# Optimization experiments

Measured on AMD Instinct MI355X. Metric: run time of the kernel, lower is better.

The kernel has to match this reference:

```python
import math
import jax, jax.numpy as jnp
import numpy as np

N_QO_HEADS = 32
N_KV_HEADS = 8
HEAD_DIM = 128
PAGE = 16          # tokens per cache block
NUM_BLOCKS = 512   # total blocks in KV cache
B = 2              # num sequences
SEQ = 2048         # tokens per sequence (q_len == kv_len, prefill)
T = B * SEQ        # total tokens


def setup_inputs() -> dict:
    key = jax.random.key(0)
    ks = jax.random.split(key, 5)
    query = jax.random.normal(ks[0], (T, N_QO_HEADS * HEAD_DIM), dtype=jnp.float32)
    k_new = jax.random.normal(ks[1], (T, N_KV_HEADS * HEAD_DIM), dtype=jnp.float32)
    v_new = jax.random.normal(ks[2], (T, N_KV_HEADS * HEAD_DIM), dtype=jnp.float32)
    key_cache = jax.random.normal(ks[3], (NUM_BLOCKS, PAGE, N_KV_HEADS, HEAD_DIM), dtype=jnp.float32)
    value_cache = jax.random.normal(ks[4], (NUM_BLOCKS, PAGE, N_KV_HEADS, HEAD_DIM), dtype=jnp.float32)
    nb = SEQ // PAGE
    block_tables = jnp.arange(B * nb, dtype=jnp.int32).reshape(B, nb)
    new_cache_slots = jnp.arange(T, dtype=jnp.int32)  # consistent with block_tables
    return {
        'query': query, 'key': k_new, 'value': v_new,
        'key_cache': key_cache, 'value_cache': value_cache,
        'block_tables': block_tables, 'new_cache_slots': new_cache_slots,
    }


def reference(query, key, value, key_cache, value_cache, block_tables, new_cache_slots):
    T_, _ = query.shape
    q = query.reshape(T_, N_QO_HEADS, HEAD_DIM)
    k_new = key.reshape(T_, N_KV_HEADS, HEAD_DIM)
    v_new = value.reshape(T_, N_KV_HEADS, HEAD_DIM)

    # set_kv_cache: scatter new K/V into the paged cache at new_cache_slots
    kc = key_cache.reshape(NUM_BLOCKS * PAGE, N_KV_HEADS, HEAD_DIM).at[new_cache_slots].set(k_new)
    vc = value_cache.reshape(NUM_BLOCKS * PAGE, N_KV_HEADS, HEAD_DIM).at[new_cache_slots].set(v_new)

    # paged gather: per-sequence token indices from block tables
    nb = block_tables.shape[1]
    idx = (block_tables[:, :, None] * PAGE + jnp.arange(PAGE, dtype=jnp.int32)[None, None, :]).reshape(B, SEQ)
    k = kc[idx]  # [B, S, Hkv, d]
    v = vc[idx]  # [B, S, Hkv, d]

    g = N_QO_HEADS // N_KV_HEADS
    qb = q.reshape(B, SEQ, N_KV_HEADS, g, HEAD_DIM)
    sm_scale = 1.0 / math.sqrt(HEAD_DIM)
    scores = jnp.einsum('bqhgd,bkhd->bhgqk', qb, k) * sm_scale  # [B,Hkv,g,S,S]

    # causal mask (q_len == kv_len so mask is k > q)
    causal = jnp.tril(jnp.ones((SEQ, SEQ), dtype=bool))
    scores = jnp.where(causal, scores, -jnp.inf)
    p = jax.nn.softmax(scores, axis=-1)
    o = jnp.einsum('bhgqk,bkhd->bqhgd', p, v)  # [B,S,Hkv,g,d]
    out = o.reshape(T_, N_QO_HEADS * HEAD_DIM).astype(query.dtype)
    return out
```

## Files before the change

### kernel.cpp

```cpp
#include <hip/hip_runtime.h>
#include <cstdint>

#define HQ 32
#define HKV 8
#define D 128
#define PAGE 16
#define SEQB 2048
#define NB 2
#define NBT (SEQB/PAGE)
#define NSLOTS (512*16)

#define BM 32
#define BN 64

typedef __bf16 bf16;
typedef __bf16 bf16x8 __attribute__((ext_vector_type(8)));
typedef float  f32x4  __attribute__((ext_vector_type(4)));

typedef __attribute__((address_space(3))) uint32_t lds_u32_t;
typedef __attribute__((address_space(1))) uint32_t glb_u32_t;

__device__ __forceinline__ void gload16(const bf16* g, bf16* l) {
    __builtin_amdgcn_global_load_lds((const glb_u32_t*)g, (lds_u32_t*)l, 16, 0, 0);
}

__global__ __launch_bounds__(256) void build_inv(const int* __restrict__ slots,
                                                 int* __restrict__ inv) {
    int t = blockIdx.x * 256 + threadIdx.x;
    if (t < NB * SEQB) inv[slots[t]] = t;
}

__global__ __launch_bounds__(256) void pack_kv(
    const float* __restrict__ knew, const float* __restrict__ vnew,
    const float* __restrict__ kc,   const float* __restrict__ vc,
    const int* __restrict__ btab,   const int* __restrict__ inv,
    bf16* __restrict__ Kp, bf16* __restrict__ Vp)
{
    int gid = blockIdx.x;
    if (gid < 2048) {
        int i   = gid*256 + threadIdx.x;
        int d8  = i & 15;
        int sg  = (i >> 4) & (SEQB - 1);
        int hkv = (i >> 15) & 7;
        int b   = i >> 18;
        int phys = btab[b*NBT + (sg >> 4)] * PAGE + (sg & 15);
        int t    = inv[phys];
        const float* src = (t >= 0 ? knew + (size_t)t * (HKV*D)
                                   : kc   + (size_t)phys * (HKV*D)) + hkv*D + d8*8;
        float4 f0 = *(const float4*)src;
        float4 f1 = *(const float4*)(src + 4);
        bf16x8 o;
        o[0]=(bf16)f0.x; o[1]=(bf16)f0.y; o[2]=(bf16)f0.z; o[3]=(bf16)f0.w;
        o[4]=(bf16)f1.x; o[5]=(bf16)f1.y; o[6]=(bf16)f1.z; o[7]=(bf16)f1.w;
        *(bf16x8*)(Kp + ((size_t)(b*HKV + hkv)*SEQB + sg)*D + d8*8) = o;
    } else {
        int i   = (gid - 2048)*256 + threadIdx.x;
        int d   = i & 127;
        int tg  = (i >> 7) & 255;
        int hkv = (i >> 15) & 7;
        int b   = i >> 18;
        int base = (tg >> 3) * 64 + ((tg >> 2) & 1) * 32 + (tg & 3) * 4;
        bf16x8 o;
        #pragma unroll
        for (int u = 0; u < 8; ++u) {
            int sg   = base + (u & 3) + ((u >> 2) << 4);
            int phys = btab[b*NBT + (sg >> 4)] * PAGE + (sg & 15);
            int t    = inv[phys];
            float v = (t >= 0) ? vnew[(size_t)t * (HKV*D) + hkv*D + d]
                               : vc  [(size_t)phys * (HKV*D) + hkv*D + d];
            o[u] = (bf16)v;
        }
        *(bf16x8*)(Vp + ((size_t)(b*HKV + hkv)*D + d)*SEQB + tg*8) = o;
    }
}

__global__ __launch_bounds__(256, 2) void attn(
    const float* __restrict__ q,
    const bf16* __restrict__ Kp,
    const bf16* __restrict__ Vp,
    float* __restrict__ out)
{
    __shared__ bf16 KT[2][BN * D];
    __shared__ bf16 VT[2][BN * D];

    const int hkv = blockIdx.x >> 5;
    const int vq  = blockIdx.x & 31;
    const int b   = blockIdx.y;

    const int tid  = threadIdx.x;
    const int w    = tid >> 6;
    const int lane = tid & 63;
    const int c    = lane & 15;
    const int quad = lane >> 4;
    const int hq   = hkv*4 + w;

    const bf16* Kbase = Kp + (size_t)(b*HKV + hkv) * SEQB * D;
    const bf16* Vbase = Vp + (size_t)(b*HKV + hkv) * (size_t)D * SEQB;

    const float CS = 0.08838834764831845f * 1.4426950408889634f;

    int kgo[4], vgo[4];
    #pragma unroll
    for (int it = 0; it < 4; ++it) {
        int o   = tid + it*256;
        int tok = o >> 4, sl = o & 15;
        int g   = (sl & 8) | ((sl & 7) ^ (tok & 7));
        kgo[it] = tok*D + g*8;
        int d = o >> 3, s2 = o & 7;
        int tg = s2 ^ (d & 7);
        vgo[it] = d*SEQB + tg*8;
    }

    int cur = 0;
    #pragma unroll
    for (int it = 0; it < 4; ++it) gload16(Kbase + kgo[it], &KT[0][(tid + it*256)*8]);
    #pragma unroll
    for (int it = 0; it < 4; ++it) gload16(Vbase + vgo[it], &VT[0][(tid + it*256)*8]);

    #pragma unroll 1
    for (int pass = 0; pass < 2; ++pass) {
        const int qt = pass ? vq : 63 - vq;

        bf16x8 qf[2][4];
        #pragma unroll
        for (int u = 0; u < 2; ++u) {
            const float* qrow = q + (size_t)(b*SEQB + qt*BM + u*16 + c) * (HQ*D) + hq*D;
            #pragma unroll
            for (int kk = 0; kk < 4; ++kk) {
                float4 f0 = *(const float4*)(qrow + kk*32 + quad*8);
                float4 f1 = *(const float4*)(qrow + kk*32 + quad*8 + 4);
                bf16x8 a;
                a[0]=(bf16)(f0.x*CS); a[1]=(bf16)(f0.y*CS); a[2]=(bf16)(f0.z*CS); a[3]=(bf16)(f0.w*CS);
                a[4]=(bf16)(f1.x*CS); a[5]=(bf16)(f1.y*CS); a[6]=(bf16)(f1.z*CS); a[7]=(bf16)(f1.w*CS);
                qf[u][kk] = a;
            }
        }

        float lrun[2];
        f32x4 accO[2][8];
        lrun[0] = 0.f; lrun[1] = 0.f;
        #pragma unroll
        for (int u = 0; u < 2; ++u)
            #pragma unroll
            for (int dt = 0; dt < 8; ++dt) accO[u][dt] = (f32x4){0.f,0.f,0.f,0.f};

        const int jmax  = (qt*BM + BM - 1) >> 6;
        const int qrow0 = qt*BM + c;

        for (int j = 0; j <= jmax; ++j) {
            __syncthreads();

            if (j < jmax) {
                const bf16* kgp = Kbase + (size_t)(j+1)*BN*D;
                const bf16* vgp = Vbase + (j+1)*BN;
                #pragma unroll
                for (int it = 0; it < 4; ++it) gload16(kgp + kgo[it], &KT[cur^1][(tid + it*256)*8]);
                #pragma unroll
                for (int it = 0; it < 4; ++it) gload16(vgp + vgo[it], &VT[cur^1][(tid + it*256)*8]);
            } else if (pass == 0) {
                #pragma unroll
                for (int it = 0; it < 4; ++it) gload16(Kbase + kgo[it], &KT[cur^1][(tid + it*256)*8]);
                #pragma unroll
                for (int it = 0; it < 4; ++it) gload16(Vbase + vgo[it], &VT[cur^1][(tid + it*256)*8]);
            }

            const bf16* Kt = KT[cur];
            const bf16* Vt = VT[cur];
            const int kb0  = j * BN;
            const bool diag = (j == jmax);

            uint32_t pw[2][4][2];
            #pragma unroll
            for (int nt = 0; nt < 4; ++nt) {
                const int tok = nt*16 + c;
                f32x4 s0 = (f32x4){0.f,0.f,0.f,0.f};
                f32x4 s1 = (f32x4){0.f,0.f,0.f,0.f};
                __builtin_amdgcn_s_setprio(1);
                #pragma unroll
                for (int kk = 0; kk < 4; ++kk) {
                    int sl = ((kk & 2) << 2) | (((kk & 1) * 4 + quad) ^ (tok & 7));
                    bf16x8 kb = *(const bf16x8*)(Kt + tok*D + sl*8);
                    s0 = __builtin_amdgcn_mfma_f32_16x16x32_bf16(kb, qf[0][kk], s0, 0, 0, 0);
                    s1 = __builtin_amdgcn_mfma_f32_16x16x32_bf16(kb, qf[1][kk], s1, 0, 0, 0);
                }
                __builtin_amdgcn_s_setprio(0);
                const int tokg = kb0 + nt*16 + quad*4;
                #pragma unroll
                for (int u = 0; u < 2; ++u) {
                    f32x4 sv = u ? s1 : s0;
                    float p0 = __builtin_amdgcn_exp2f(sv[0]);
                    float p1 = __builtin_amdgcn_exp2f(sv[1]);
                    float p2 = __builtin_amdgcn_exp2f(sv[2]);
                    float p3 = __builtin_amdgcn_exp2f(sv[3]);
                    if (diag) {
                        const int qr = qrow0 + u*16;
                        if (tokg     > qr) p0 = 0.0f;
                        if (tokg + 1 > qr) p1 = 0.0f;
                        if (tokg + 2 > qr) p2 = 0.0f;
                        if (tokg + 3 > qr) p3 = 0.0f;
                    }
                    lrun[u] += (p0 + p1) + (p2 + p3);
                    asm("v_cvt_pk_bf16_f32 %0, %1, %2" : "=v"(pw[u][nt][0]) : "v"(p0), "v"(p1));
                    asm("v_cvt_pk_bf16_f32 %0, %1, %2" : "=v"(pw[u][nt][1]) : "v"(p2), "v"(p3));
                }
            }

            union PA { uint32_t w[4]; bf16x8 v; };
            PA pa00, pa01, pa10, pa11;
            pa00.w[0]=pw[0][0][0]; pa00.w[1]=pw[0][0][1]; pa00.w[2]=pw[0][1][0]; pa00.w[3]=pw[0][1][1];
            pa01.w[0]=pw[0][2][0]; pa01.w[1]=pw[0][2][1]; pa01.w[2]=pw[0][3][0]; pa01.w[3]=pw[0][3][1];
            pa10.w[0]=pw[1][0][0]; pa10.w[1]=pw[1][0][1]; pa10.w[2]=pw[1][1][0]; pa10.w[3]=pw[1][1][1];
            pa11.w[0]=pw[1][2][0]; pa11.w[1]=pw[1][2][1]; pa11.w[2]=pw[1][3][0]; pa11.w[3]=pw[1][3][1];
            const int sl0 = ((quad    ) ^ (c & 7)) * 8;
            const int sl1 = ((quad + 4) ^ (c & 7)) * 8;
            __builtin_amdgcn_s_setprio(1);
            #pragma unroll
            for (int dt = 0; dt < 8; ++dt) {
                const bf16* vrow = Vt + (size_t)(dt*16 + c) * BN;
                bf16x8 vb0 = *(const bf16x8*)(vrow + sl0);
                accO[0][dt] = __builtin_amdgcn_mfma_f32_16x16x32_bf16(pa00.v, vb0, accO[0][dt], 0, 0, 0);
                accO[1][dt] = __builtin_amdgcn_mfma_f32_16x16x32_bf16(pa10.v, vb0, accO[1][dt], 0, 0, 0);
                bf16x8 vb1 = *(const bf16x8*)(vrow + sl1);
                accO[0][dt] = __builtin_amdgcn_mfma_f32_16x16x32_bf16(pa01.v, vb1, accO[0][dt], 0, 0, 0);
                accO[1][dt] = __builtin_amdgcn_mfma_f32_16x16x32_bf16(pa11.v, vb1, accO[1][dt], 0, 0, 0);
            }
            __builtin_amdgcn_s_setprio(0);

            cur ^= 1;
        }

        #pragma unroll
        for (int u = 0; u < 2; ++u) {
            float l = lrun[u];
            l += __shfl_xor(l, 16);
            l += __shfl_xor(l, 32);
            #pragma unroll
            for (int rr = 0; rr < 4; ++rr) {
                float lr = __shfl(l, quad*4 + rr);
                float inv = 1.0f / lr;
                float* orow = out + (size_t)(b*SEQB + qt*BM + u*16 + quad*4 + rr) * (HQ*D) + hq*D;
                #pragma unroll
                for (int dt = 0; dt < 8; ++dt)
                    orow[dt*16 + c] = accO[u][dt][rr] * inv;
            }
        }
    }
}

extern "C" void kernel_launch(void* const* d_in, const int* in_sizes, int n_in,
                              void* d_out, int out_size, void* d_ws, size_t ws_size,
                              hipStream_t stream) {
    const float* q     = (const float*)d_in[0];
    const float* knew  = (const float*)d_in[1];
    const float* vnew  = (const float*)d_in[2];
    const float* kc    = (const float*)d_in[3];
    const float* vc    = (const float*)d_in[4];
    const int*   btab  = (const int*)d_in[5];
    const int*   slots = (const int*)d_in[6];
    float*       out   = (float*)d_out;

    int*  inv = (int*)d_ws;
    bf16* Kp  = (bf16*)((char*)d_ws + 65536);
    bf16* Vp  = Kp + (size_t)NB * HKV * SEQB * D;

    hipMemsetAsync(inv, 0xFF, NSLOTS * sizeof(int), stream);
    build_inv<<<(NB*SEQB + 255)/256, 256, 0, stream>>>(slots, inv);
    pack_kv<<<4096, 256, 0, stream>>>(knew, vnew, kc, vc, btab, inv, Kp, Vp);

    dim3 grid(8 * 32, NB);
    attn<<<grid, 256, 0, stream>>>(q, Kp, Vp, out);
}
```

Measured before the change: 257.9 us.

## Single-buffer K in LDS, one q-tile per block, raise occupancy to 3

K drops to a single LDS buffer while V keeps two. The next K/V load is issued only after the QK^T phase, behind explicit vmcnt waits and raw barriers. The two-pass pairing of q-tiles per block is removed: the grid doubles to one q-tile per block, ordered longest-first with heads interleaved. Launch bounds ask for 3 blocks per CU. The aim is more resident blocks and better load balance, at the cost of less prefetch distance for K and possible register pressure.

```diff
diff --git a/kernel.cpp b/kernel.cpp
--- a/kernel.cpp
+++ b/kernel.cpp
@@ -74,17 +74,17 @@
     }
 }
 
-__global__ __launch_bounds__(256, 2) void attn(
+__global__ __launch_bounds__(256, 3) void attn(
     const float* __restrict__ q,
     const bf16* __restrict__ Kp,
     const bf16* __restrict__ Vp,
     float* __restrict__ out)
 {
-    __shared__ bf16 KT[2][BN * D];
+    __shared__ bf16 Kt[BN * D];
     __shared__ bf16 VT[2][BN * D];
 
-    const int hkv = blockIdx.x >> 5;
-    const int vq  = blockIdx.x & 31;
+    const int hkv = blockIdx.x & 7;
+    const int qt  = 63 - (blockIdx.x >> 3);
     const int b   = blockIdx.y;
 
     const int tid  = threadIdx.x;
@@ -111,138 +111,134 @@
         vgo[it] = d*SEQB + tg*8;
     }
 
-    int cur = 0;
-    #pragma unroll
-    for (int it = 0; it < 4; ++it) gload16(Kbase + kgo[it], &KT[0][(tid + it*256)*8]);
+    #pragma unroll
+    for (int it = 0; it < 4; ++it) gload16(Kbase + kgo[it], &Kt[(tid + it*256)*8]);
     #pragma unroll
     for (int it = 0; it < 4; ++it) gload16(Vbase + vgo[it], &VT[0][(tid + it*256)*8]);
 
-    #pragma unroll 1
-    for (int pass = 0; pass < 2; ++pass) {
-        const int qt = pass ? vq : 63 - vq;
-
-        bf16x8 qf[2][4];
-        #pragma unroll
-        for (int u = 0; u < 2; ++u) {
-            const float* qrow = q + (size_t)(b*SEQB + qt*BM + u*16 + c) * (HQ*D) + hq*D;
+    bf16x8 qf[2][4];
+    #pragma unroll
+    for (int u = 0; u < 2; ++u) {
+        const float* qrow = q + (size_t)(b*SEQB + qt*BM + u*16 + c) * (HQ*D) + hq*D;
+        #pragma unroll
+        for (int kk = 0; kk < 4; ++kk) {
+            float4 f0 = *(const float4*)(qrow + kk*32 + quad*8);
+            float4 f1 = *(const float4*)(qrow + kk*32 + quad*8 + 4);
+            bf16x8 a;
+            a[0]=(bf16)(f0.x*CS); a[1]=(bf16)(f0.y*CS); a[2]=(bf16)(f0.z*CS); a[3]=(bf16)(f0.w*CS);
+            a[4]=(bf16)(f1.x*CS); a[5]=(bf16)(f1.y*CS); a[6]=(bf16)(f1.z*CS); a[7]=(bf16)(f1.w*CS);
+            qf[u][kk] = a;
+        }
+    }
+
+    float lrun[2];
+    f32x4 accO[2][8];
+    lrun[0] = 0.f; lrun[1] = 0.f;
+    #pragma unroll
+    for (int u = 0; u < 2; ++u)
+        #pragma unroll
+        for (int dt = 0; dt < 8; ++dt) accO[u][dt] = (f32x4){0.f,0.f,0.f,0.f};
+
+    const int jmax  = (qt*BM + BM - 1) >> 6;
+    const int qrow0 = qt*BM + c;
+    int vcur = 0;
+
+    for (int j = 0; j <= jmax; ++j) {
+        asm volatile("s_waitcnt vmcnt(4)" ::: "memory");
+        __builtin_amdgcn_s_barrier();
+        __builtin_amdgcn_sched_barrier(0);
+
+        const int kb0  = j * BN;
+        const bool diag = (j == jmax);
+
+        uint32_t pw[2][4][2];
+        #pragma unroll
+        for (int nt = 0; nt < 4; ++nt) {
+            const int tok = nt*16 + c;
+            f32x4 s0 = (f32x4){0.f,0.f,0.f,0.f};
+            f32x4 s1 = (f32x4){0.f,0.f,0.f,0.f};
+            __builtin_amdgcn_s_setprio(1);
             #pragma unroll
             for (int kk = 0; kk < 4; ++kk) {
-                float4 f0 = *(const float4*)(qrow + kk*32 + quad*8);
-                float4 f1 = *(const float4*)(qrow + kk*32 + quad*8 + 4);
-                bf16x8 a;
-                a[0]=(bf16)(f0.x*CS); a[1]=(bf16)(f0.y*CS); a[2]=(bf16)(f0.z*CS); a[3]=(bf16)(f0.w*CS);
-                a[4]=(bf16)(f1.x*CS); a[5]=(bf16)(f1.y*CS); a[6]=(bf16)(f1.z*CS); a[7]=(bf16)(f1.w*CS);
-                qf[u][kk] = a;
-            }
-        }
-
-        float lrun[2];
-        f32x4 accO[2][8];
-        lrun[0] = 0.f; lrun[1] = 0.f;
-        #pragma unroll
-        for (int u = 0; u < 2; ++u)
-            #pragma unroll
-            for (int dt = 0; dt < 8; ++dt) accO[u][dt] = (f32x4){0.f,0.f,0.f,0.f};
-
-        const int jmax  = (qt*BM + BM - 1) >> 6;
-        const int qrow0 = qt*BM + c;
-
-        for (int j = 0; j <= jmax; ++j) {
-            __syncthreads();
-
-            if (j < jmax) {
-                const bf16* kgp = Kbase + (size_t)(j+1)*BN*D;
-                const bf16* vgp = Vbase + (j+1)*BN;
-                #pragma unroll
-                for (int it = 0; it < 4; ++it) gload16(kgp + kgo[it], &KT[cur^1][(tid + it*256)*8]);
-                #pragma unroll
-                for (int it = 0; it < 4; ++it) gload16(vgp + vgo[it], &VT[cur^1][(tid + it*256)*8]);
-            } else if (pass == 0) {
-                #pragma unroll
-                for (int it = 0; it < 4; ++it) gload16(Kbase + kgo[it], &KT[cur^1][(tid + it*256)*8]);
-                #pragma unroll
-                for (int it = 0; it < 4; ++it) gload16(Vbase + vgo[it], &VT[cur^1][(tid + it*256)*8]);
-            }
-
-            const bf16* Kt = KT[cur];
-            const bf16* Vt = VT[cur];
-            const int kb0  = j * BN;
-            const bool diag = (j == jmax);
-
-            uint32_t pw[2][4][2];
-            #pragma unroll
-            for (int nt = 0; nt < 4; ++nt) {
-                const int tok = nt*16 + c;
-                f32x4 s0 = (f32x4){0.f,0.f,0.f,0.f};
-                f32x4 s1 = (f32x4){0.f,0.f,0.f,0.f};
-                __builtin_amdgcn_s_setprio(1);
-                #pragma unroll
-                for (int kk = 0; kk < 4; ++kk) {
-                    int sl = ((kk & 2) << 2) | (((kk & 1) * 4 + quad) ^ (tok & 7));
-                    bf16x8 kb = *(const bf16x8*)(Kt + tok*D + sl*8);
-                    s0 = __builtin_amdgcn_mfma_f32_16x16x32_bf16(kb, qf[0][kk], s0, 0, 0, 0);
-                    s1 = __builtin_amdgcn_mfma_f32_16x16x32_bf16(kb, qf[1][kk], s1, 0, 0, 0);
-                }
-                __builtin_amdgcn_s_setprio(0);
-                const int tokg = kb0 + nt*16 + quad*4;
-                #pragma unroll
-                for (int u = 0; u < 2; ++u) {
-                    f32x4 sv = u ? s1 : s0;
-                    float p0 = __builtin_amdgcn_exp2f(sv[0]);
-                    float p1 = __builtin_amdgcn_exp2f(sv[1]);
-                    float p2 = __builtin_amdgcn_exp2f(sv[2]);
-                    float p3 = __builtin_amdgcn_exp2f(sv[3]);
-                    if (diag) {
-                        const int qr = qrow0 + u*16;
-                        if (tokg     > qr) p0 = 0.0f;
-                        if (tokg + 1 > qr) p1 = 0.0f;
-                        if (tokg + 2 > qr) p2 = 0.0f;
-                        if (tokg + 3 > qr) p3 = 0.0f;
-                    }
-                    lrun[u] += (p0 + p1) + (p2 + p3);
-                    asm("v_cvt_pk_bf16_f32 %0, %1, %2" : "=v"(pw[u][nt][0]) : "v"(p0), "v"(p1));
-                    asm("v_cvt_pk_bf16_f32 %0, %1, %2" : "=v"(pw[u][nt][1]) : "v"(p2), "v"(p3));
-                }
-            }
-
-            union PA { uint32_t w[4]; bf16x8 v; };
-            PA pa00, pa01, pa10, pa11;
-            pa00.w[0]=pw[0][0][0]; pa00.w[1]=pw[0][0][1]; pa00.w[2]=pw[0][1][0]; pa00.w[3]=pw[0][1][1];
-            pa01.w[0]=pw[0][2][0]; pa01.w[1]=pw[0][2][1]; pa01.w[2]=pw[0][3][0]; pa01.w[3]=pw[0][3][1];
-            pa10.w[0]=pw[1][0][0]; pa10.w[1]=pw[1][0][1]; pa10.w[2]=pw[1][1][0]; pa10.w[3]=pw[1][1][1];
-            pa11.w[0]=pw[1][2][0]; pa11.w[1]=pw[1][2][1]; pa11.w[2]=pw[1][3][0]; pa11.w[3]=pw[1][3][1];
-            const int sl0 = ((quad    ) ^ (c & 7)) * 8;
-            const int sl1 = ((quad + 4) ^ (c & 7)) * 8;
-            __builtin_amdgcn_s_setprio(1);
-            #pragma unroll
-            for (int dt = 0; dt < 8; ++dt) {
-                const bf16* vrow = Vt + (size_t)(dt*16 + c) * BN;
-                bf16x8 vb0 = *(const bf16x8*)(vrow + sl0);
-                accO[0][dt] = __builtin_amdgcn_mfma_f32_16x16x32_bf16(pa00.v, vb0, accO[0][dt], 0, 0, 0);
-                accO[1][dt] = __builtin_amdgcn_mfma_f32_16x16x32_bf16(pa10.v, vb0, accO[1][dt], 0, 0, 0);
-                bf16x8 vb1 = *(const bf16x8*)(vrow + sl1);
-                accO[0][dt] = __builtin_amdgcn_mfma_f32_16x16x32_bf16(pa01.v, vb1, accO[0][dt], 0, 0, 0);
-                accO[1][dt] = __builtin_amdgcn_mfma_f32_16x16x32_bf16(pa11.v, vb1, accO[1][dt], 0, 0, 0);
+                int sl = ((kk & 2) << 2) | (((kk & 1) * 4 + quad) ^ (tok & 7));
+                bf16x8 kb = *(const bf16x8*)(Kt + tok*D + sl*8);
+                s0 = __builtin_amdgcn_mfma_f32_16x16x32_bf16(kb, qf[0][kk], s0, 0, 0, 0);
+                s1 = __builtin_amdgcn_mfma_f32_16x16x32_bf16(kb, qf[1][kk], s1, 0, 0, 0);
             }
             __builtin_amdgcn_s_setprio(0);
-
-            cur ^= 1;
-        }
-
-        #pragma unroll
-        for (int u = 0; u < 2; ++u) {
-            float l = lrun[u];
-            l += __shfl_xor(l, 16);
-            l += __shfl_xor(l, 32);
-            #pragma unroll
-            for (int rr = 0; rr < 4; ++rr) {
-                float lr = __shfl(l, quad*4 + rr);
-                float inv = 1.0f / lr;
-                float* orow = out + (size_t)(b*SEQB + qt*BM + u*16 + quad*4 + rr) * (HQ*D) + hq*D;
-                #pragma unroll
-                for (int dt = 0; dt < 8; ++dt)
-                    orow[dt*16 + c] = accO[u][dt][rr] * inv;
+            const int tokg = kb0 + nt*16 + quad*4;
+            #pragma unroll
+            for (int u = 0; u < 2; ++u) {
+                f32x4 sv = u ? s1 : s0;
+                float p0 = __builtin_amdgcn_exp2f(sv[0]);
+                float p1 = __builtin_amdgcn_exp2f(sv[1]);
+                float p2 = __builtin_amdgcn_exp2f(sv[2]);
+                float p3 = __builtin_amdgcn_exp2f(sv[3]);
+                if (diag) {
+                    const int qr = qrow0 + u*16;
+                    if (tokg     > qr) p0 = 0.0f;
+                    if (tokg + 1 > qr) p1 = 0.0f;
+                    if (tokg + 2 > qr) p2 = 0.0f;
+                    if (tokg + 3 > qr) p3 = 0.0f;
+                }
+                lrun[u] += (p0 + p1) + (p2 + p3);
+                asm("v_cvt_pk_bf16_f32 %0, %1, %2" : "=v"(pw[u][nt][0]) : "v"(p0), "v"(p1));
+                asm("v_cvt_pk_bf16_f32 %0, %1, %2" : "=v"(pw[u][nt][1]) : "v"(p2), "v"(p3));
             }
+        }
+
+        asm volatile("s_waitcnt vmcnt(0)" ::: "memory");
+        __builtin_amdgcn_s_barrier();
+        __builtin_amdgcn_sched_barrier(0);
+
+        if (j < jmax) {
+            const bf16* kgp = Kbase + (size_t)(j+1)*BN*D;
+            const bf16* vgp = Vbase + (j+1)*BN;
+            #pragma unroll
+            for (int it = 0; it < 4; ++it) gload16(kgp + kgo[it], &Kt[(tid + it*256)*8]);
+            #pragma unroll
+            for (int it = 0; it < 4; ++it) gload16(vgp + vgo[it], &VT[vcur^1][(tid + it*256)*8]);
+        }
+
+        const bf16* Vt = VT[vcur];
+
+        union PA { uint32_t w[4]; bf16x8 v; };
+        PA pa00, pa01, pa10, pa11;
+        pa00.w[0]=pw[0][0][0]; pa00.w[1]=pw[0][0][1]; pa00.w[2]=pw[0][1][0]; pa00.w[3]=pw[0][1][1];
+        pa01.w[0]=pw[0][2][0]; pa01.w[1]=pw[0][2][1]; pa01.w[2]=pw[0][3][0]; pa01.w[3]=pw[0][3][1];
+        pa10.w[0]=pw[1][0][0]; pa10.w[1]=pw[1][0][1]; pa10.w[2]=pw[1][1][0]; pa10.w[3]=pw[1][1][1];
+        pa11.w[0]=pw[1][2][0]; pa11.w[1]=pw[1][2][1]; pa11.w[2]=pw[1][3][0]; pa11.w[3]=pw[1][3][1];
+        const int sl0 = ((quad    ) ^ (c & 7)) * 8;
+        const int sl1 = ((quad + 4) ^ (c & 7)) * 8;
+        __builtin_amdgcn_s_setprio(1);
+        #pragma unroll
+        for (int dt = 0; dt < 8; ++dt) {
+            const bf16* vrow = Vt + (size_t)(dt*16 + c) * BN;
+            bf16x8 vb0 = *(const bf16x8*)(vrow + sl0);
+            accO[0][dt] = __builtin_amdgcn_mfma_f32_16x16x32_bf16(pa00.v, vb0, accO[0][dt], 0, 0, 0);
+            accO[1][dt] = __builtin_amdgcn_mfma_f32_16x16x32_bf16(pa10.v, vb0, accO[1][dt], 0, 0, 0);
+            bf16x8 vb1 = *(const bf16x8*)(vrow + sl1);
+            accO[0][dt] = __builtin_amdgcn_mfma_f32_16x16x32_bf16(pa01.v, vb1, accO[0][dt], 0, 0, 0);
+            accO[1][dt] = __builtin_amdgcn_mfma_f32_16x16x32_bf16(pa11.v, vb1, accO[1][dt], 0, 0, 0);
+        }
+        __builtin_amdgcn_s_setprio(0);
+
+        vcur ^= 1;
+    }
+
+    #pragma unroll
+    for (int u = 0; u < 2; ++u) {
+        float l = lrun[u];
+        l += __shfl_xor(l, 16);
+        l += __shfl_xor(l, 32);
+        #pragma unroll
+        for (int rr = 0; rr < 4; ++rr) {
+            float lr = __shfl(l, quad*4 + rr);
+            float inv = 1.0f / lr;
+            float* orow = out + (size_t)(b*SEQB + qt*BM + u*16 + quad*4 + rr) * (HQ*D) + hq*D;
+            #pragma unroll
+            for (int dt = 0; dt < 8; ++dt)
+                orow[dt*16 + c] = accO[u][dt][rr] * inv;
         }
     }
 }
@@ -267,6 +263,6 @@
     build_inv<<<(NB*SEQB + 255)/256, 256, 0, stream>>>(slots, inv);
     pack_kv<<<4096, 256, 0, stream>>>(knew, vnew, kc, vc, btab, inv, Kp, Vp);
 
-    dim3 grid(8 * 32, NB);
+    dim3 grid(8 * 64, NB);
     attn<<<grid, 256, 0, stream>>>(q, Kp, Vp, out);
 }
```

Result: slower. 263.1 us (+2.0%).
